# Kernel optimization log

Hardware: AMD Instinct MI355X
Metric: run time of the kernel (lower is better)

Reference implementation:

```python
import jax, jax.numpy as jnp
import numpy as np

B, N, M = 8, 8192, 2048
C1, C2 = 128, 256
H = 256  # mlp hidden/out channels


def setup_inputs() -> dict:
    key = jax.random.key(0)
    ks = jax.random.split(key, 8)
    return {
        "unknown": jax.random.normal(ks[0], (B, N, 3), dtype=jnp.float32),
        "known": jax.random.normal(ks[1], (B, M, 3), dtype=jnp.float32),
        "unknow_feats": jax.random.normal(ks[2], (B, C1, N), dtype=jnp.float32),
        "known_feats": jax.random.normal(ks[3], (B, C2, M), dtype=jnp.float32),
        "W1": jax.random.normal(ks[4], (H, C1 + C2), dtype=jnp.float32) * 0.02,
        "b1": jnp.zeros((H,), dtype=jnp.float32),
        "W2": jax.random.normal(ks[5], (H, H), dtype=jnp.float32) * 0.02,
        "b2": jnp.zeros((H,), dtype=jnp.float32),
    }


def _three_nn(unknown, known):
    # squared pairwise distances (B, n, m)
    d2 = jnp.sum((unknown[:, :, None, :] - known[:, None, :, :]) ** 2, axis=-1)
    neg_d2_top, idx = jax.lax.top_k(-d2, 3)  # 3 smallest distances
    dist = jnp.sqrt(jnp.maximum(-neg_d2_top, 0.0))  # (B, n, 3)
    return dist, idx


def _three_interpolate(features, idx, weight):
    # features: (B, c, m); idx, weight: (B, n, 3) -> (B, c, n)
    Bc, c, m = features.shape
    n = idx.shape[1]
    idx_flat = jnp.broadcast_to(idx.reshape(Bc, 1, n * 3), (Bc, c, n * 3))
    gathered = jnp.take_along_axis(features, idx_flat, axis=2).reshape(Bc, c, n, 3)
    return jnp.sum(gathered * weight[:, None, :, :], axis=-1)


def reference(unknown, known, unknow_feats, known_feats, W1, b1, W2, b2):
    dist, idx = _three_nn(unknown, known)
    dist_recip = 1.0 / (dist + 1e-8)
    weight = dist_recip / jnp.sum(dist_recip, axis=2, keepdims=True)  # (B, n, 3)
    interpolated = _three_interpolate(known_feats, idx, weight)  # (B, C2, n)
    new_features = jnp.concatenate([interpolated, unknow_feats], axis=1)  # (B, C1+C2, n)
    # shared MLP: two conv1x1 (bias, no BN) + ReLU
    h = jax.nn.relu(jnp.einsum('oc,bcn->bon', W1, new_features) + b1[None, :, None])
    out = jax.nn.relu(jnp.einsum('oc,bcn->bon', W2, h) + b2[None, :, None])
    return out
```

## Files before the change

kernel.cpp:

```cpp
#include <hip/hip_runtime.h>

using bf16x8 = __attribute__((ext_vector_type(8))) short;
using f32x4  = __attribute__((ext_vector_type(4))) float;

constexpr int Bb = 8, Nn = 8192, Mm = 2048, C1 = 128, C2 = 256, Hh = 256, K1 = 384;
constexpr int KT1 = K1 / 32;
constexpr int KT2 = Hh / 32;
constexpr int RT = Hh / 16;

__device__ __forceinline__ short f2bf(float x) {
  union { float f; unsigned u; } v; v.f = x;
  unsigned r = v.u + 0x7fff + ((v.u >> 16) & 1);
  return (short)(r >> 16);
}

__global__ __launch_bounds__(256) void transpose_k(const float* __restrict__ src,
                                                   float* __restrict__ dst, int R, int C) {
  __shared__ float tile[32][33];
  size_t off = (size_t)blockIdx.z * R * C;
  src += off; dst += off;
  int c0 = blockIdx.x * 32, r0 = blockIdx.y * 32;
  int tx = threadIdx.x, ty = threadIdx.y;
#pragma unroll
  for (int rr = ty; rr < 32; rr += 8) tile[rr][tx] = src[(size_t)(r0 + rr) * C + c0 + tx];
  __syncthreads();
#pragma unroll
  for (int cc = ty; cc < 32; cc += 8) dst[(size_t)(c0 + cc) * R + r0 + tx] = tile[tx][cc];
}

__global__ __launch_bounds__(256) void prep_w_k(const float* __restrict__ W1,
                                                const float* __restrict__ W2,
                                                short* __restrict__ W1f,
                                                short* __restrict__ W2f) {
  int id = blockIdx.x * 256 + threadIdx.x;
  const int n1 = KT1 * RT * 64;
  const int n2 = KT2 * RT * 64;
  if (id < n1) {
    int lane = id & 63, tile = id >> 6;
    int kt = tile / RT, rt = tile % RT;
    int m = rt * 16 + (lane & 15), k0 = kt * 32 + (lane >> 4) * 8;
    bf16x8 f;
#pragma unroll
    for (int j = 0; j < 8; ++j) f[j] = f2bf(W1[(size_t)m * K1 + k0 + j]);
    *(bf16x8*)(W1f + (size_t)id * 8) = f;
  } else if (id < n1 + n2) {
    int id2 = id - n1;
    int lane = id2 & 63, tile = id2 >> 6;
    int kt = tile / RT, rt = tile % RT;
    int m = rt * 16 + (lane & 15), k0 = kt * 32 + (lane >> 4) * 8;
    bf16x8 f;
#pragma unroll
    for (int j = 0; j < 8; ++j) f[j] = f2bf(W2[(size_t)m * Hh + k0 + j]);
    *(bf16x8*)(W2f + (size_t)id2 * 8) = f;
  }
}

__global__ __launch_bounds__(256) void nn_half_k(const float* __restrict__ unknown,
                                                 const float* __restrict__ known,
                                                 float* __restrict__ pd,
                                                 int* __restrict__ pi) {
  __shared__ float kx[1024], ky[1024], kz[1024];
  int bid = blockIdx.x;
  int b = bid >> 6, rem = bid & 63;
  int half = rem & 1, nblk = rem >> 1;
  int n = nblk * 256 + threadIdx.x;
  const float* kb = known + ((size_t)b * Mm + half * 1024) * 3;
  for (int p = threadIdx.x; p < 1024; p += 256) {
    kx[p] = kb[3 * p]; ky[p] = kb[3 * p + 1]; kz[p] = kb[3 * p + 2];
  }
  __syncthreads();

  size_t ui = ((size_t)b * Nn + n) * 3;
  float ux = unknown[ui], uy = unknown[ui + 1], uz = unknown[ui + 2];
  float d0 = 1e30f, d1 = 1e30f, d2 = 1e30f;
  int i0 = 0, i1 = 0, i2 = 0;
  int gbase = half * 1024;

#define NN_STEP(xx, yy, zz, q)                                          \
  {                                                                     \
    float dx = ux - (xx), dy = uy - (yy), dz = uz - (zz);               \
    float dd = dx * dx + dy * dy + dz * dz;                             \
    if (__any(dd < d2)) {    \
      int jm = gbase + jb + (q);                                        \
      bool c0 = dd < d0, c1 = dd < d1, c2 = dd < d2;                    \
      d2 = c1 ? d1 : (c2 ? dd : d2); i2 = c1 ? i1 : (c2 ? jm : i2);     \
      d1 = c0 ? d0 : (c1 ? dd : d1); i1 = c0 ? i0 : (c1 ? jm : i1);     \
      d0 = c0 ? dd : d0;             i0 = c0 ? jm : i0;                 \
    }                                                                   \
  }

  for (int jb = 0; jb < 1024; jb += 4) {
    float4 xs = *(const float4*)&kx[jb];
    float4 ys = *(const float4*)&ky[jb];
    float4 zs = *(const float4*)&kz[jb];
    NN_STEP(xs.x, ys.x, zs.x, 0)
    NN_STEP(xs.y, ys.y, zs.y, 1)
    NN_STEP(xs.z, ys.z, zs.z, 2)
    NN_STEP(xs.w, ys.w, zs.w, 3)
  }
#undef NN_STEP

  size_t o = (((size_t)b * Nn + n) * 2 + half) * 3;
  pd[o] = d0; pd[o + 1] = d1; pd[o + 2] = d2;
  pi[o] = i0; pi[o + 1] = i1; pi[o + 2] = i2;
}

__global__ __launch_bounds__(256) void nn_merge_k(const float* __restrict__ pd,
                                                  const int* __restrict__ pi,
                                                  int* __restrict__ idx3,
                                                  float* __restrict__ w3) {
  int t = blockIdx.x * 256 + threadIdx.x;
  size_t o = (size_t)t * 6;
  float a0 = pd[o], a1 = pd[o + 1], a2 = pd[o + 2];
  float b0 = pd[o + 3], b1v = pd[o + 4], b2v = pd[o + 5];
  int A0 = pi[o], A1 = pi[o + 1], A2 = pi[o + 2];
  int B0 = pi[o + 3], B1 = pi[o + 4], B2 = pi[o + 5];
  bool ta = a0 <= b0;
  float m0 = ta ? a0 : b0; int j0 = ta ? A0 : B0;
  float na0 = ta ? a1 : a0, na1 = ta ? a2 : a1;
  int   nA0 = ta ? A1 : A0, nA1 = ta ? A2 : A1;
  float nb0 = ta ? b0 : b1v, nb1 = ta ? b1v : b2v;
  int   nB0 = ta ? B0 : B1,  nB1 = ta ? B1 : B2;
  ta = na0 <= nb0;
  float m1 = ta ? na0 : nb0; int j1 = ta ? nA0 : nB0;
  float ma0 = ta ? na1 : na0; int mA0 = ta ? nA1 : nA0;
  float mb0 = ta ? nb0 : nb1; int mB0 = ta ? nB0 : nB1;
  ta = ma0 <= mb0;
  float m2 = ta ? ma0 : mb0; int j2 = ta ? mA0 : mB0;

  float s0 = sqrtf(m0), s1 = sqrtf(m1), s2 = sqrtf(m2);
  float r0 = 1.f / (s0 + 1e-8f), r1 = 1.f / (s1 + 1e-8f), r2 = 1.f / (s2 + 1e-8f);
  float rs = 1.f / (r0 + r1 + r2);
  size_t ui = (size_t)t * 3;
  idx3[ui] = j0; idx3[ui + 1] = j1; idx3[ui + 2] = j2;
  w3[ui] = r0 * rs; w3[ui + 1] = r1 * rs; w3[ui + 2] = r2 * rs;
}

__global__ __launch_bounds__(256) void fused_gemm_k(
    const float* __restrict__ uf, const float* __restrict__ kfT,
    const short* __restrict__ W1f, const float* __restrict__ b1,
    const short* __restrict__ W2f, const float* __restrict__ b2,
    const int* __restrict__ idx3, const float* __restrict__ w3,
    float* __restrict__ out) {
  __shared__ short Fs[KT1 * 4 * 64 * 8];
  __shared__ short Hs[KT2 * 4 * 64 * 8];
  int bid = blockIdx.x;
  int b = bid >> 7, bt = bid & 127;
  int tid = threadIdx.x, lane = tid & 63, wv = tid >> 6;
  int quad = lane >> 4, col = lane & 15;

  {
    int n = bt * 64 + wv * 16 + col;
    size_t o3 = ((size_t)b * Nn + n) * 3;
    int g0 = idx3[o3], g1 = idx3[o3 + 1], g2 = idx3[o3 + 2];
    float w0 = w3[o3], w1 = w3[o3 + 1], w2 = w3[o3 + 2];
    const float* kfb = kfT + (size_t)b * Mm * C2;
#pragma unroll 2
    for (int kt = 0; kt < 8; ++kt) {
      int c0 = kt * 32 + quad * 8;
      float4 p0a = *(const float4*)&kfb[(size_t)g0 * C2 + c0];
      float4 p0b = *(const float4*)&kfb[(size_t)g0 * C2 + c0 + 4];
      float4 p1a = *(const float4*)&kfb[(size_t)g1 * C2 + c0];
      float4 p1b = *(const float4*)&kfb[(size_t)g1 * C2 + c0 + 4];
      float4 p2a = *(const float4*)&kfb[(size_t)g2 * C2 + c0];
      float4 p2b = *(const float4*)&kfb[(size_t)g2 * C2 + c0 + 4];
      bf16x8 f;
      f[0] = f2bf(w0 * p0a.x + w1 * p1a.x + w2 * p2a.x);
      f[1] = f2bf(w0 * p0a.y + w1 * p1a.y + w2 * p2a.y);
      f[2] = f2bf(w0 * p0a.z + w1 * p1a.z + w2 * p2a.z);
      f[3] = f2bf(w0 * p0a.w + w1 * p1a.w + w2 * p2a.w);
      f[4] = f2bf(w0 * p0b.x + w1 * p1b.x + w2 * p2b.x);
      f[5] = f2bf(w0 * p0b.y + w1 * p1b.y + w2 * p2b.y);
      f[6] = f2bf(w0 * p0b.z + w1 * p1b.z + w2 * p2b.z);
      f[7] = f2bf(w0 * p0b.w + w1 * p1b.w + w2 * p2b.w);
      *(bf16x8*)&Fs[((kt * 4 + wv) * 64 + lane) * 8] = f;
    }
#pragma unroll 2
    for (int kt = 8; kt < 12; ++kt) {
      int c1 = (kt - 8) * 32 + quad * 8;
      bf16x8 f;
#pragma unroll
      for (int j = 0; j < 8; ++j)
        f[j] = f2bf(uf[((size_t)b * C1 + c1 + j) * Nn + n]);
      *(bf16x8*)&Fs[((kt * 4 + wv) * 64 + lane) * 8] = f;
    }
  }
  __syncthreads();

  f32x4 acc[4][4];
#pragma unroll
  for (int r = 0; r < 4; ++r)
#pragma unroll
    for (int c = 0; c < 4; ++c) acc[r][c] = (f32x4){0.f, 0.f, 0.f, 0.f};

  for (int kt = 0; kt < KT1; ++kt) {
    bf16x8 Afr[4], Bfr[4];
#pragma unroll
    for (int r = 0; r < 4; ++r)
      Afr[r] = *(const bf16x8*)(W1f + ((size_t)(kt * RT + wv * 4 + r) * 64 + lane) * 8);
#pragma unroll
    for (int c = 0; c < 4; ++c)
      Bfr[c] = *(const bf16x8*)&Fs[((kt * 4 + c) * 64 + lane) * 8];
#pragma unroll
    for (int r = 0; r < 4; ++r)
#pragma unroll
      for (int c = 0; c < 4; ++c)
        acc[r][c] = __builtin_amdgcn_mfma_f32_16x16x32_bf16(Afr[r], Bfr[c], acc[r][c], 0, 0, 0);
  }

#pragma unroll
  for (int r = 0; r < 4; ++r) {
    f32x4 bq = *(const f32x4*)&b1[wv * 64 + r * 16 + quad * 4];
#pragma unroll
    for (int c = 0; c < 4; ++c)
#pragma unroll
      for (int reg = 0; reg < 4; ++reg)
        acc[r][c][reg] = fmaxf(acc[r][c][reg] + bq[reg], 0.f);
  }
  {
    int addr_lo = (((quad & 1) * 2) * 16 + col) * 4;
    bool hiSel = lane >= 32;
#pragma unroll
    for (int ktl = 0; ktl < 2; ++ktl)
#pragma unroll
      for (int c = 0; c < 4; ++c) {
        bf16x8 f;
#pragma unroll
        for (int j = 0; j < 8; ++j) {
          int addr = addr_lo + (j >> 2) * 64;
          int lo = __builtin_amdgcn_ds_bpermute(addr, __float_as_int(acc[ktl * 2][c][j & 3]));
          int hi = __builtin_amdgcn_ds_bpermute(addr, __float_as_int(acc[ktl * 2 + 1][c][j & 3]));
          f[j] = f2bf(__int_as_float(hiSel ? hi : lo));
        }
        *(bf16x8*)&Hs[(((wv * 2 + ktl) * 4 + c) * 64 + lane) * 8] = f;
      }
  }
  __syncthreads();

  f32x4 acc2[4][4];
#pragma unroll
  for (int r = 0; r < 4; ++r)
#pragma unroll
    for (int c = 0; c < 4; ++c) acc2[r][c] = (f32x4){0.f, 0.f, 0.f, 0.f};

  for (int kt = 0; kt < KT2; ++kt) {
    bf16x8 Afr[4], Bfr[4];
#pragma unroll
    for (int r = 0; r < 4; ++r)
      Afr[r] = *(const bf16x8*)(W2f + ((size_t)(kt * RT + wv * 4 + r) * 64 + lane) * 8);
#pragma unroll
    for (int c = 0; c < 4; ++c)
      Bfr[c] = *(const bf16x8*)&Hs[((kt * 4 + c) * 64 + lane) * 8];
#pragma unroll
    for (int r = 0; r < 4; ++r)
#pragma unroll
      for (int c = 0; c < 4; ++c)
        acc2[r][c] = __builtin_amdgcn_mfma_f32_16x16x32_bf16(Afr[r], Bfr[c], acc2[r][c], 0, 0, 0);
  }

#pragma unroll
  for (int r = 0; r < 4; ++r) {
    f32x4 bq = *(const f32x4*)&b2[wv * 64 + r * 16 + quad * 4];
#pragma unroll
    for (int c = 0; c < 4; ++c)
#pragma unroll
      for (int reg = 0; reg < 4; ++reg) {
        int rowg = wv * 64 + r * 16 + quad * 4 + reg;
        int n = bt * 64 + c * 16 + col;
        out[((size_t)b * Hh + rowg) * Nn + n] = fmaxf(acc2[r][c][reg] + bq[reg], 0.f);
      }
  }
}

extern "C" void kernel_launch(void* const* d_in, const int* in_sizes, int n_in,
                              void* d_out, int out_size, void* d_ws, size_t ws_size,
                              hipStream_t stream) {
  const float* unknown = (const float*)d_in[0];
  const float* known   = (const float*)d_in[1];
  const float* uf      = (const float*)d_in[2];
  const float* kf      = (const float*)d_in[3];
  const float* W1      = (const float*)d_in[4];
  const float* b1      = (const float*)d_in[5];
  const float* W2      = (const float*)d_in[6];
  const float* b2      = (const float*)d_in[7];
  float* out = (float*)d_out;

  char* p = (char*)d_ws;
  float* kfT = (float*)p;  p += (size_t)Bb * Mm * C2 * 4;
  int* idx3  = (int*)p;    p += (size_t)Bb * Nn * 3 * 4;
  float* w3  = (float*)p;  p += (size_t)Bb * Nn * 3 * 4;
  short* W1f = (short*)p;  p += (size_t)KT1 * RT * 64 * 8 * 2;
  short* W2f = (short*)p;  p += (size_t)KT2 * RT * 64 * 8 * 2;
  float* pd  = (float*)p;  p += (size_t)Bb * Nn * 2 * 3 * 4;
  int* pi    = (int*)p;    p += (size_t)Bb * Nn * 2 * 3 * 4;

  transpose_k<<<dim3(Mm / 32, C2 / 32, Bb), dim3(32, 8), 0, stream>>>(kf, kfT, C2, Mm);
  prep_w_k<<<dim3((KT1 * RT * 64 + KT2 * RT * 64) / 256), dim3(256), 0, stream>>>(W1, W2, W1f, W2f);
  nn_half_k<<<dim3(Bb * 64), dim3(256), 0, stream>>>(unknown, known, pd, pi);
  nn_merge_k<<<dim3(Bb * Nn / 256), dim3(256), 0, stream>>>(pd, pi, idx3, w3);
  fused_gemm_k<<<dim3(Bb * (Nn / 64)), dim3(256), 0, stream>>>(
      uf, kfT, W1f, b1, W2f, b2, idx3, w3, out);
}
```

Before: 241.1 us.

## Split kNN search into quarters, fuse merge into GEMM, combine prep kernels

The nearest-neighbour search now splits the known points into four quarters instead of two, doubling the block count to 1024 for better GPU occupancy. The separate merge kernel is removed: the fused GEMM kernel loads the four partial top-3 lists, merges them and computes the interpolation weights inline. The transpose and weight-prep kernels are combined into one launch. This cuts two kernel launches and the idx/weight round trip through memory, at the cost of larger partial buffers and extra merge work inside the GEMM kernel.

```diff
diff --git a/kernel.cpp b/kernel.cpp
--- a/kernel.cpp
+++ b/kernel.cpp
@@ -7,6 +7,8 @@
 constexpr int KT1 = K1 / 32;
 constexpr int KT2 = Hh / 32;
 constexpr int RT = Hh / 16;
+constexpr int NQ = 4;
+constexpr int MQ = Mm / NQ;
 
 __device__ __forceinline__ short f2bf(float x) {
   union { float f; unsigned u; } v; v.f = x;
@@ -14,30 +16,52 @@
   return (short)(r >> 16);
 }
 
-__global__ __launch_bounds__(256) void transpose_k(const float* __restrict__ src,
-                                                   float* __restrict__ dst, int R, int C) {
+__device__ __forceinline__ void merge3(float a0, float a1, float a2, int A0, int A1, int A2,
+                                       float b0, float b1, float b2, int B0, int B1, int B2,
+                                       float& m0, float& m1, float& m2,
+                                       int& j0, int& j1, int& j2) {
+  bool ta = a0 <= b0;
+  m0 = ta ? a0 : b0; j0 = ta ? A0 : B0;
+  float na0 = ta ? a1 : a0, na1 = ta ? a2 : a1;
+  int   nA0 = ta ? A1 : A0, nA1 = ta ? A2 : A1;
+  float nb0 = ta ? b0 : b1, nb1 = ta ? b1 : b2;
+  int   nB0 = ta ? B0 : B1, nB1 = ta ? B1 : B2;
+  ta = na0 <= nb0;
+  m1 = ta ? na0 : nb0; j1 = ta ? nA0 : nB0;
+  float ma0 = ta ? na1 : na0; int mA0 = ta ? nA1 : nA0;
+  float mb0 = ta ? nb0 : nb1; int mB0 = ta ? nB0 : nB1;
+  ta = ma0 <= mb0;
+  m2 = ta ? ma0 : mb0; j2 = ta ? mA0 : mB0;
+}
+
+__global__ __launch_bounds__(256) void prep_all_k(const float* __restrict__ kf,
+                                                  float* __restrict__ kfT,
+                                                  const float* __restrict__ W1,
+                                                  const float* __restrict__ W2,
+                                                  short* __restrict__ W1f,
+                                                  short* __restrict__ W2f) {
   __shared__ float tile[32][33];
-  size_t off = (size_t)blockIdx.z * R * C;
-  src += off; dst += off;
-  int c0 = blockIdx.x * 32, r0 = blockIdx.y * 32;
-  int tx = threadIdx.x, ty = threadIdx.y;
-#pragma unroll
-  for (int rr = ty; rr < 32; rr += 8) tile[rr][tx] = src[(size_t)(r0 + rr) * C + c0 + tx];
-  __syncthreads();
-#pragma unroll
-  for (int cc = ty; cc < 32; cc += 8) dst[(size_t)(c0 + cc) * R + r0 + tx] = tile[tx][cc];
-}
-
-__global__ __launch_bounds__(256) void prep_w_k(const float* __restrict__ W1,
-                                                const float* __restrict__ W2,
-                                                short* __restrict__ W1f,
-                                                short* __restrict__ W2f) {
-  int id = blockIdx.x * 256 + threadIdx.x;
+  int bid = blockIdx.x, tid = threadIdx.x;
+  if (bid < 4096) {
+    int cx = bid & 63, ry = (bid >> 6) & 7, z = bid >> 9;
+    const int R = C2, C = Mm;
+    const float* src = kf + (size_t)z * R * C;
+    float* dst = kfT + (size_t)z * R * C;
+    int c0 = cx * 32, r0 = ry * 32;
+    int tx = tid & 31, ty = tid >> 5;
+#pragma unroll
+    for (int rr = ty; rr < 32; rr += 8) tile[rr][tx] = src[(size_t)(r0 + rr) * C + c0 + tx];
+    __syncthreads();
+#pragma unroll
+    for (int cc = ty; cc < 32; cc += 8) dst[(size_t)(c0 + cc) * R + r0 + tx] = tile[tx][cc];
+    return;
+  }
+  int id = (bid - 4096) * 256 + tid;
   const int n1 = KT1 * RT * 64;
   const int n2 = KT2 * RT * 64;
   if (id < n1) {
-    int lane = id & 63, tile = id >> 6;
-    int kt = tile / RT, rt = tile % RT;
+    int lane = id & 63, t = id >> 6;
+    int kt = t / RT, rt = t % RT;
     int m = rt * 16 + (lane & 15), k0 = kt * 32 + (lane >> 4) * 8;
     bf16x8 f;
 #pragma unroll
@@ -45,8 +69,8 @@
     *(bf16x8*)(W1f + (size_t)id * 8) = f;
   } else if (id < n1 + n2) {
     int id2 = id - n1;
-    int lane = id2 & 63, tile = id2 >> 6;
-    int kt = tile / RT, rt = tile % RT;
+    int lane = id2 & 63, t = id2 >> 6;
+    int kt = t / RT, rt = t % RT;
     int m = rt * 16 + (lane & 15), k0 = kt * 32 + (lane >> 4) * 8;
     bf16x8 f;
 #pragma unroll
@@ -55,17 +79,17 @@
   }
 }
 
-__global__ __launch_bounds__(256) void nn_half_k(const float* __restrict__ unknown,
-                                                 const float* __restrict__ known,
-                                                 float* __restrict__ pd,
-                                                 int* __restrict__ pi) {
-  __shared__ float kx[1024], ky[1024], kz[1024];
+__global__ __launch_bounds__(256) void nn_quarter_k(const float* __restrict__ unknown,
+                                                    const float* __restrict__ known,
+                                                    float* __restrict__ pd,
+                                                    int* __restrict__ pi) {
+  __shared__ float kx[MQ], ky[MQ], kz[MQ];
   int bid = blockIdx.x;
-  int b = bid >> 6, rem = bid & 63;
-  int half = rem & 1, nblk = rem >> 1;
+  int b = bid >> 7, rem = bid & 127;
+  int q = rem & 3, nblk = rem >> 2;
   int n = nblk * 256 + threadIdx.x;
-  const float* kb = known + ((size_t)b * Mm + half * 1024) * 3;
-  for (int p = threadIdx.x; p < 1024; p += 256) {
+  const float* kb = known + ((size_t)b * Mm + q * MQ) * 3;
+  for (int p = threadIdx.x; p < MQ; p += 256) {
     kx[p] = kb[3 * p]; ky[p] = kb[3 * p + 1]; kz[p] = kb[3 * p + 2];
   }
   __syncthreads();
@@ -74,14 +98,14 @@
   float ux = unknown[ui], uy = unknown[ui + 1], uz = unknown[ui + 2];
   float d0 = 1e30f, d1 = 1e30f, d2 = 1e30f;
   int i0 = 0, i1 = 0, i2 = 0;
-  int gbase = half * 1024;
-
-#define NN_STEP(xx, yy, zz, q)                                          \
+  int gbase = q * MQ;
+
+#define NN_STEP(xx, yy, zz, qq)                                         \
   {                                                                     \
     float dx = ux - (xx), dy = uy - (yy), dz = uz - (zz);               \
     float dd = dx * dx + dy * dy + dz * dz;                             \
     if (__any(dd < d2)) {    \
-      int jm = gbase + jb + (q);                                        \
+      int jm = gbase + jb + (qq);                                       \
       bool c0 = dd < d0, c1 = dd < d1, c2 = dd < d2;                    \
       d2 = c1 ? d1 : (c2 ? dd : d2); i2 = c1 ? i1 : (c2 ? jm : i2);     \
       d1 = c0 ? d0 : (c1 ? dd : d1); i1 = c0 ? i0 : (c1 ? jm : i1);     \
@@ -89,7 +113,7 @@
     }                                                                   \
   }
 
-  for (int jb = 0; jb < 1024; jb += 4) {
+  for (int jb = 0; jb < MQ; jb += 4) {
     float4 xs = *(const float4*)&kx[jb];
     float4 ys = *(const float4*)&ky[jb];
     float4 zs = *(const float4*)&kz[jb];
@@ -100,47 +124,16 @@
   }
 #undef NN_STEP
 
-  size_t o = (((size_t)b * Nn + n) * 2 + half) * 3;
+  size_t o = (((size_t)b * Nn + n) * NQ + q) * 3;
   pd[o] = d0; pd[o + 1] = d1; pd[o + 2] = d2;
   pi[o] = i0; pi[o + 1] = i1; pi[o + 2] = i2;
-}
-
-__global__ __launch_bounds__(256) void nn_merge_k(const float* __restrict__ pd,
-                                                  const int* __restrict__ pi,
-                                                  int* __restrict__ idx3,
-                                                  float* __restrict__ w3) {
-  int t = blockIdx.x * 256 + threadIdx.x;
-  size_t o = (size_t)t * 6;
-  float a0 = pd[o], a1 = pd[o + 1], a2 = pd[o + 2];
-  float b0 = pd[o + 3], b1v = pd[o + 4], b2v = pd[o + 5];
-  int A0 = pi[o], A1 = pi[o + 1], A2 = pi[o + 2];
-  int B0 = pi[o + 3], B1 = pi[o + 4], B2 = pi[o + 5];
-  bool ta = a0 <= b0;
-  float m0 = ta ? a0 : b0; int j0 = ta ? A0 : B0;
-  float na0 = ta ? a1 : a0, na1 = ta ? a2 : a1;
-  int   nA0 = ta ? A1 : A0, nA1 = ta ? A2 : A1;
-  float nb0 = ta ? b0 : b1v, nb1 = ta ? b1v : b2v;
-  int   nB0 = ta ? B0 : B1,  nB1 = ta ? B1 : B2;
-  ta = na0 <= nb0;
-  float m1 = ta ? na0 : nb0; int j1 = ta ? nA0 : nB0;
-  float ma0 = ta ? na1 : na0; int mA0 = ta ? nA1 : nA0;
-  float mb0 = ta ? nb0 : nb1; int mB0 = ta ? nB0 : nB1;
-  ta = ma0 <= mb0;
-  float m2 = ta ? ma0 : mb0; int j2 = ta ? mA0 : mB0;
-
-  float s0 = sqrtf(m0), s1 = sqrtf(m1), s2 = sqrtf(m2);
-  float r0 = 1.f / (s0 + 1e-8f), r1 = 1.f / (s1 + 1e-8f), r2 = 1.f / (s2 + 1e-8f);
-  float rs = 1.f / (r0 + r1 + r2);
-  size_t ui = (size_t)t * 3;
-  idx3[ui] = j0; idx3[ui + 1] = j1; idx3[ui + 2] = j2;
-  w3[ui] = r0 * rs; w3[ui + 1] = r1 * rs; w3[ui + 2] = r2 * rs;
 }
 
 __global__ __launch_bounds__(256) void fused_gemm_k(
     const float* __restrict__ uf, const float* __restrict__ kfT,
     const short* __restrict__ W1f, const float* __restrict__ b1,
     const short* __restrict__ W2f, const float* __restrict__ b2,
-    const int* __restrict__ idx3, const float* __restrict__ w3,
+    const float* __restrict__ pd, const int* __restrict__ pi,
     float* __restrict__ out) {
   __shared__ short Fs[KT1 * 4 * 64 * 8];
   __shared__ short Hs[KT2 * 4 * 64 * 8];
@@ -151,9 +144,26 @@
 
   {
     int n = bt * 64 + wv * 16 + col;
-    size_t o3 = ((size_t)b * Nn + n) * 3;
-    int g0 = idx3[o3], g1 = idx3[o3 + 1], g2 = idx3[o3 + 2];
-    float w0 = w3[o3], w1 = w3[o3 + 1], w2 = w3[o3 + 2];
+    size_t pbase = (size_t)(b * Nn + n) * (NQ * 3);
+    float4 da = *(const float4*)&pd[pbase];
+    float4 db = *(const float4*)&pd[pbase + 4];
+    float4 dc = *(const float4*)&pd[pbase + 8];
+    int4 ia = *(const int4*)&pi[pbase];
+    int4 ib = *(const int4*)&pi[pbase + 4];
+    int4 ic = *(const int4*)&pi[pbase + 8];
+    float t0, t1, t2, u0, u1, u2, m0, m1, m2;
+    int T0, T1, T2, U0, U1, U2, g0, g1, g2;
+    merge3(da.x, da.y, da.z, ia.x, ia.y, ia.z,
+           da.w, db.x, db.y, ia.w, ib.x, ib.y, t0, t1, t2, T0, T1, T2);
+    merge3(db.z, db.w, dc.x, ib.z, ib.w, ic.x,
+           dc.y, dc.z, dc.w, ic.y, ic.z, ic.w, u0, u1, u2, U0, U1, U2);
+    merge3(t0, t1, t2, T0, T1, T2, u0, u1, u2, U0, U1, U2,
+           m0, m1, m2, g0, g1, g2);
+    float s0 = sqrtf(m0), s1 = sqrtf(m1), s2 = sqrtf(m2);
+    float r0 = 1.f / (s0 + 1e-8f), r1 = 1.f / (s1 + 1e-8f), r2 = 1.f / (s2 + 1e-8f);
+    float rs = 1.f / (r0 + r1 + r2);
+    float w0 = r0 * rs, w1 = r1 * rs, w2 = r2 * rs;
+
     const float* kfb = kfT + (size_t)b * Mm * C2;
 #pragma unroll 2
     for (int kt = 0; kt < 8; ++kt) {
@@ -287,17 +297,14 @@
 
   char* p = (char*)d_ws;
   float* kfT = (float*)p;  p += (size_t)Bb * Mm * C2 * 4;
-  int* idx3  = (int*)p;    p += (size_t)Bb * Nn * 3 * 4;
-  float* w3  = (float*)p;  p += (size_t)Bb * Nn * 3 * 4;
   short* W1f = (short*)p;  p += (size_t)KT1 * RT * 64 * 8 * 2;
   short* W2f = (short*)p;  p += (size_t)KT2 * RT * 64 * 8 * 2;
-  float* pd  = (float*)p;  p += (size_t)Bb * Nn * 2 * 3 * 4;
-  int* pi    = (int*)p;    p += (size_t)Bb * Nn * 2 * 3 * 4;
-
-  transpose_k<<<dim3(Mm / 32, C2 / 32, Bb), dim3(32, 8), 0, stream>>>(kf, kfT, C2, Mm);
-  prep_w_k<<<dim3((KT1 * RT * 64 + KT2 * RT * 64) / 256), dim3(256), 0, stream>>>(W1, W2, W1f, W2f);
-  nn_half_k<<<dim3(Bb * 64), dim3(256), 0, stream>>>(unknown, known, pd, pi);
-  nn_merge_k<<<dim3(Bb * Nn / 256), dim3(256), 0, stream>>>(pd, pi, idx3, w3);
+  float* pd  = (float*)p;  p += (size_t)Bb * Nn * NQ * 3 * 4;
+  int* pi    = (int*)p;    p += (size_t)Bb * Nn * NQ * 3 * 4;
+
+  const int prep_blocks = 4096 + (KT1 * RT * 64 + KT2 * RT * 64 + 255) / 256;
+  prep_all_k<<<dim3(prep_blocks), dim3(256), 0, stream>>>(kf, kfT, W1, W2, W1f, W2f);
+  nn_quarter_k<<<dim3(Bb * 32 * NQ), dim3(256), 0, stream>>>(unknown, known, pd, pi);
   fused_gemm_k<<<dim3(Bb * (Nn / 64)), dim3(256), 0, stream>>>(
-      uf, kfT, W1f, b1, W2f, b2, idx3, w3, out);
-}
+      uf, kfT, W1f, b1, W2f, b2, pd, pi, out);
+}
```

Result: faster. 223.5 us (-7.3%).
